# Performance work log

Measured on AMD Instinct MI355X. Metric: run time of the kernel, lower is better.

Reference implementation:

```python
import jax, jax.numpy as jnp
import numpy as np

HEADS = 8
DIM_HEAD = 64
LN_EPS = 1e-5


def _layernorm(x, gamma, beta):
    mu = jnp.mean(x, axis=-1, keepdims=True)
    var = jnp.var(x, axis=-1, keepdims=True)
    return (x - mu) * jax.lax.rsqrt(var + LN_EPS) * gamma + beta


def setup_inputs() -> dict:
    key = jax.random.key(0)
    ks = jax.random.split(key, 5)
    B, N, D = 1, 16384, 512
    return {
        "x": jax.random.normal(ks[0], (B, N, D), dtype=jnp.float32),
        "ln_gamma": jnp.ones((D,), dtype=jnp.float32),
        "ln_beta": jnp.zeros((D,), dtype=jnp.float32),
        "w_qkv": jax.random.normal(ks[1], (D, 3 * D), dtype=jnp.float32) * (D ** -0.5),
        "agent": jax.random.normal(ks[2], (HEADS, 512, DIM_HEAD), dtype=jnp.float32) * (DIM_HEAD ** -0.5),
        "w_out": jax.random.normal(ks[3], (D, D), dtype=jnp.float32) * (D ** -0.5),
        "b_out": jnp.zeros((D,), dtype=jnp.float32),
    }


def reference(x, ln_gamma, ln_beta, w_qkv, agent, w_out, b_out):
    # TransLayer: x + Mask_Agent_Attention(LayerNorm(x))
    B, N, D = x.shape
    xn = _layernorm(x, ln_gamma, ln_beta)

    qkv = xn @ w_qkv                                   # [B, N, 3D]
    q, k, v = jnp.split(qkv, 3, axis=-1)
    # [B, H, N, d]
    q = q.reshape(B, N, HEADS, DIM_HEAD).transpose(0, 2, 1, 3)
    k = k.reshape(B, N, HEADS, DIM_HEAD).transpose(0, 2, 1, 3)
    v = v.reshape(B, N, HEADS, DIM_HEAD).transpose(0, 2, 1, 3)

    scale = DIM_HEAD ** -0.5  # tem=0 -> classical 1/sqrt(d) scaling

    # agents aggregate values: softmax over keys  [B, H, A, N]
    attn1 = jax.nn.softmax(jnp.einsum('had,bhnd->bhan', agent, k) * scale, axis=-1)
    agent_v = jnp.einsum('bhan,bhnd->bhad', attn1, v)  # [B, H, A, d]

    # queries attend to agents: softmax over agents  [B, H, N, A]
    attn2 = jax.nn.softmax(jnp.einsum('bhnd,had->bhna', q, agent) * scale, axis=-1)
    out = jnp.einsum('bhna,bhad->bhnd', attn2, agent_v)  # [B, H, N, d]

    out = out + v  # residual=True: value residual inside attention
    out = out.transpose(0, 2, 1, 3).reshape(B, N, D)
    out = out @ w_out + b_out
    return x + out
```

## Files before the change

kernel.cpp:

```cpp
#include <hip/hip_runtime.h>
#include <stdint.h>

typedef unsigned short u16;
typedef __attribute__((ext_vector_type(8))) short bf16x8;
typedef __attribute__((ext_vector_type(4))) float f32x4;

__device__ __forceinline__ float bf2f(u16 u){
  union { uint32_t i; float f; } v; v.i = ((uint32_t)u) << 16; return v.f;
}
__device__ __forceinline__ u16 f2bf(float f){
  union { float fl; uint32_t i; } v; v.fl = f;
  uint32_t r = v.i + 0x7FFFu + ((v.i >> 16) & 1u);
  return (u16)(r >> 16);
}
__device__ __forceinline__ uint32_t cvt_pk_bf16(float lo, float hi){
  uint32_t r;
  asm("v_cvt_pk_bf16_f32 %0, %1, %2" : "=v"(r) : "v"(lo), "v"(hi));
  return r;
}
__device__ __forceinline__ f32x4 mfma16(bf16x8 a, bf16x8 b, f32x4 c){
  return __builtin_amdgcn_mfma_f32_16x16x32_bf16(a, b, c, 0, 0, 0);
}
__device__ __forceinline__ void gload16(const u16* g, u16* l){
  __builtin_amdgcn_global_load_lds((const __attribute__((address_space(1))) void*)g,
                                   (__attribute__((address_space(3))) void*)l, 16, 0, 0);
}

__global__ __launch_bounds__(256) void k_conv_bf(const float* __restrict__ in, u16* __restrict__ out, int n, float scale){
  int i = (blockIdx.x * 256 + threadIdx.x) * 4;
  if (i >= n) return;
  float4 v = *(const float4*)(in + i);
  ushort4 o; o.x=f2bf(v.x*scale); o.y=f2bf(v.y*scale); o.z=f2bf(v.z*scale); o.w=f2bf(v.w*scale);
  *(ushort4*)(out + i) = o;
}

__global__ __launch_bounds__(256) void k_transp(const float* __restrict__ in, u16* __restrict__ out, int R, int C){
  __shared__ u16 tile[64][68];
  int c0 = blockIdx.x * 64, r0 = blockIdx.y * 64;
  int tr = threadIdx.x >> 4;
  int tc = (threadIdx.x & 15) * 4;
  for (int rr = 0; rr < 4; rr++){
    int r = rr * 16 + tr;
    float4 v = *(const float4*)(in + (size_t)(r0 + r) * C + c0 + tc);
    ushort4 o; o.x=f2bf(v.x); o.y=f2bf(v.y); o.z=f2bf(v.z); o.w=f2bf(v.w);
    *(ushort4*)&tile[r][tc] = o;
  }
  __syncthreads();
  for (int rr = 0; rr < 4; rr++){
    int oc = rr * 16 + tr;
    ushort4 o;
    o.x = tile[tc+0][oc]; o.y = tile[tc+1][oc]; o.z = tile[tc+2][oc]; o.w = tile[tc+3][oc];
    *(ushort4*)(out + (size_t)(c0 + oc) * R + r0 + tc) = o;
  }
}

__global__ __launch_bounds__(128) void k_ln(const float* __restrict__ x, const float* __restrict__ g,
                                            const float* __restrict__ b, u16* __restrict__ xn){
  int row = blockIdx.x;
  int t = threadIdx.x;
  float4 v = *(const float4*)(x + (size_t)row * 512 + t * 4);
  float s = v.x + v.y + v.z + v.w;
  float q = v.x*v.x + v.y*v.y + v.z*v.z + v.w*v.w;
  for (int o = 32; o > 0; o >>= 1){ s += __shfl_down(s, o); q += __shfl_down(q, o); }
  __shared__ float red[4];
  if ((t & 63) == 0){ red[(t >> 6) * 2] = s; red[(t >> 6) * 2 + 1] = q; }
  __syncthreads();
  float mu  = (red[0] + red[2]) * (1.0f/512.0f);
  float var = (red[1] + red[3]) * (1.0f/512.0f) - mu * mu;
  float rs = rsqrtf(var + 1e-5f);
  float4 gv = *(const float4*)(g + t * 4);
  float4 bv = *(const float4*)(b + t * 4);
  ushort4 o;
  o.x = f2bf((v.x - mu) * rs * gv.x + bv.x);
  o.y = f2bf((v.y - mu) * rs * gv.y + bv.y);
  o.z = f2bf((v.z - mu) * rs * gv.z + bv.z);
  o.w = f2bf((v.w - mu) * rs * gv.w + bv.w);
  *(ushort4*)(xn + (size_t)row * 512 + t * 4) = o;
}

__global__ __launch_bounds__(512) void k_gemm_qkv(const u16* __restrict__ A, const u16* __restrict__ Bt,
                                                  u16* __restrict__ C, u16* __restrict__ vT){
  __shared__ u16 aL[2][256 * 64];
  __shared__ u16 bL[2][128 * 64];
  int m0 = blockIdx.x * 256, n0 = blockIdx.y * 128;
  int t = threadIdx.x, w = t >> 6, l = t & 63;
  int wm = (w >> 1) * 64, wn = (w & 1) * 64;
  int lr = l & 15;
  int blkSrc = (l & 7) ^ ((l >> 3) & 7);
  const u16* gA = A  + (size_t)(m0 + w*8 + (l >> 3)) * 512 + blkSrc * 8;
  const u16* gB = Bt + (size_t)(n0 + w*8 + (l >> 3)) * 512 + blkSrc * 8;
  f32x4 acc[4][4];
  for (int i=0;i<4;i++) for (int j=0;j<4;j++) acc[i][j] = {0.f,0.f,0.f,0.f};

  auto stage = [&](int buf, int k0){
    #pragma unroll
    for (int p = 0; p < 4; p++)
      gload16(gA + (size_t)p*64*512 + k0, &aL[buf][(p*64 + w*8) * 64]);
    #pragma unroll
    for (int p = 0; p < 2; p++)
      gload16(gB + (size_t)p*64*512 + k0, &bL[buf][(p*64 + w*8) * 64]);
  };
  auto comp = [&](const u16* ab, const u16* bb){
    #pragma unroll
    for (int kk = 0; kk < 64; kk += 32){
      int xo = (((l >> 4) + (kk >> 3)) ^ (l & 7)) << 3;
      bf16x8 av[4], bv[4];
      #pragma unroll
      for (int mt=0;mt<4;mt++) av[mt] = *(const bf16x8*)&ab[(wm + mt*16 + lr)*64 + xo];
      #pragma unroll
      for (int nt=0;nt<4;nt++) bv[nt] = *(const bf16x8*)&bb[(wn + nt*16 + lr)*64 + xo];
      #pragma unroll
      for (int mt=0;mt<4;mt++)
        #pragma unroll
        for (int nt=0;nt<4;nt++)
          acc[mt][nt] = mfma16(av[mt], bv[nt], acc[mt][nt]);
    }
  };

  stage(0, 0);
  stage(1, 64);
  asm volatile("s_waitcnt vmcnt(6)" ::: "memory");
  __builtin_amdgcn_s_barrier();
  asm volatile("" ::: "memory");
  int cur = 0;
  #pragma unroll
  for (int tk = 0; tk < 8; tk++){
    comp(&aL[cur][0], &bL[cur][0]);
    if (tk < 7){
      __builtin_amdgcn_s_barrier();
      if (tk + 2 < 8){
        stage(cur, (tk + 2) * 64);
        asm volatile("s_waitcnt vmcnt(6)" ::: "memory");
      } else {
        asm volatile("s_waitcnt vmcnt(0)" ::: "memory");
      }
      __builtin_amdgcn_s_barrier();
      asm volatile("" ::: "memory");
    }
    cur ^= 1;
  }

  int rr = (l >> 4) * 4, cc = l & 15;
  bool isV = (n0 >= 1024);
  for (int mt=0;mt<4;mt++) for (int nt=0;nt<4;nt++){
    int r = m0 + wm + mt*16 + rr;
    int c = n0 + wn + nt*16 + cc;
    ushort4 o;
    o.x = f2bf(acc[mt][nt][0]); o.y = f2bf(acc[mt][nt][1]);
    o.z = f2bf(acc[mt][nt][2]); o.w = f2bf(acc[mt][nt][3]);
    C[(size_t)(r+0) * 1536 + c] = o.x;
    C[(size_t)(r+1) * 1536 + c] = o.y;
    C[(size_t)(r+2) * 1536 + c] = o.z;
    C[(size_t)(r+3) * 1536 + c] = o.w;
    if (isV) *(ushort4*)(vT + ((size_t)(c - 1024) << 14) + r) = o;
  }
}

__global__ __launch_bounds__(512) void k_gemm_out(const u16* __restrict__ A, const u16* __restrict__ Bt,
                                                  const float* __restrict__ x, const float* __restrict__ bias,
                                                  float* __restrict__ y){
  __shared__ u16 aL[2][256 * 64];
  __shared__ u16 bL[2][128 * 64];
  int m0 = blockIdx.x * 256, n0 = blockIdx.y * 128;
  int t = threadIdx.x, w = t >> 6, l = t & 63;
  int wm = (w >> 1) * 64, wn = (w & 1) * 64;
  int lr = l & 15;
  int blkSrc = (l & 7) ^ ((l >> 3) & 7);
  const u16* gA = A  + (size_t)(m0 + w*8 + (l >> 3)) * 512 + blkSrc * 8;
  const u16* gB = Bt + (size_t)(n0 + w*8 + (l >> 3)) * 512 + blkSrc * 8;
  f32x4 acc[4][4];
  for (int i=0;i<4;i++) for (int j=0;j<4;j++) acc[i][j] = {0.f,0.f,0.f,0.f};

  auto stage = [&](int buf, int k0){
    #pragma unroll
    for (int p = 0; p < 4; p++)
      gload16(gA + (size_t)p*64*512 + k0, &aL[buf][(p*64 + w*8) * 64]);
    #pragma unroll
    for (int p = 0; p < 2; p++)
      gload16(gB + (size_t)p*64*512 + k0, &bL[buf][(p*64 + w*8) * 64]);
  };
  auto comp = [&](const u16* ab, const u16* bb){
    #pragma unroll
    for (int kk = 0; kk < 64; kk += 32){
      int xo = (((l >> 4) + (kk >> 3)) ^ (l & 7)) << 3;
      bf16x8 av[4], bv[4];
      #pragma unroll
      for (int mt=0;mt<4;mt++) av[mt] = *(const bf16x8*)&ab[(wm + mt*16 + lr)*64 + xo];
      #pragma unroll
      for (int nt=0;nt<4;nt++) bv[nt] = *(const bf16x8*)&bb[(wn + nt*16 + lr)*64 + xo];
      #pragma unroll
      for (int mt=0;mt<4;mt++)
        #pragma unroll
        for (int nt=0;nt<4;nt++)
          acc[mt][nt] = mfma16(av[mt], bv[nt], acc[mt][nt]);
    }
  };

  stage(0, 0);
  stage(1, 64);
  asm volatile("s_waitcnt vmcnt(6)" ::: "memory");
  __builtin_amdgcn_s_barrier();
  asm volatile("" ::: "memory");
  int cur = 0;
  #pragma unroll
  for (int tk = 0; tk < 8; tk++){
    comp(&aL[cur][0], &bL[cur][0]);
    if (tk < 7){
      __builtin_amdgcn_s_barrier();
      if (tk + 2 < 8){
        stage(cur, (tk + 2) * 64);
        asm volatile("s_waitcnt vmcnt(6)" ::: "memory");
      } else {
        asm volatile("s_waitcnt vmcnt(0)" ::: "memory");
      }
      __builtin_amdgcn_s_barrier();
      asm volatile("" ::: "memory");
    }
    cur ^= 1;
  }

  int rr = (l >> 4) * 4, cc = l & 15;
  for (int mt=0;mt<4;mt++) for (int nt=0;nt<4;nt++)
    for (int j=0;j<4;j++){
      int r = m0 + wm + mt*16 + rr + j;
      int c = n0 + wn + nt*16 + cc;
      y[(size_t)r * 512 + c] = acc[mt][nt][j] + bias[c] + x[(size_t)r * 512 + c];
    }
}

__global__ __launch_bounds__(256) void k_agent_agg(const u16* __restrict__ agbf, const u16* __restrict__ qkv,
                                                   const u16* __restrict__ vT,
                                                   float* __restrict__ nump, float* __restrict__ denp){
  int L = blockIdx.x;
  int g = (L >> 6) * 8 + (L & 7);
  int m = (L >> 3) & 7;
  int h = g >> 4, ch = g & 15, a0 = m * 64;

  __shared__ u16 ag[64][68];
  __shared__ u16 kt[64][68];
  __shared__ u16 vt[64][68];
  __shared__ u16 pt[64][68];
  __shared__ float dnf[4][64];
  int t = threadIdx.x, w = t >> 6, l = t & 63;
  int lr = l & 15, q4 = l >> 4;

  int sr = t >> 2, sc = (t & 3) * 16;
  {
    uint4 a0v = *(const uint4*)(agbf + (size_t)(h * 512 + a0 + sr) * 64 + sc);
    uint4 a1v = *(const uint4*)(agbf + (size_t)(h * 512 + a0 + sr) * 64 + sc + 8);
    *(uint4*)&ag[sr][sc]     = a0v;
    *(uint4*)&ag[sr][sc + 8] = a1v;
  }

  size_t nbase = (size_t)ch * 1024;
  const u16* kp = qkv + 512 + h * 64;
  const u16* vp = vT + ((size_t)(h * 64 + sr) << 14);

  f32x4 acc2[4];
  #pragma unroll
  for (int i=0;i<4;i++) acc2[i] = {0.f,0.f,0.f,0.f};
  float den[4] = {0.f,0.f,0.f,0.f};

  for (int sub = 0; sub < 16; sub++){
    size_t n0 = nbase + sub * 64;
    __syncthreads();
    {
      uint4 rk0 = *(const uint4*)(kp + (n0 + sr) * 1536 + sc);
      uint4 rk1 = *(const uint4*)(kp + (n0 + sr) * 1536 + sc + 8);
      uint4 rv0 = *(const uint4*)(vp + n0 + sc);
      uint4 rv1 = *(const uint4*)(vp + n0 + sc + 8);
      *(uint4*)&kt[sr][sc]     = rk0;
      *(uint4*)&kt[sr][sc + 8] = rk1;
      *(uint4*)&vt[sr][sc]     = rv0;
      *(uint4*)&vt[sr][sc + 8] = rv1;
    }
    __syncthreads();

    f32x4 s[4];
    #pragma unroll
    for (int nt=0;nt<4;nt++) s[nt] = {0.f,0.f,0.f,0.f};
    #pragma unroll
    for (int kk = 0; kk < 64; kk += 32){
      int kb = kk + q4 * 8;
      bf16x8 kf = *(const bf16x8*)&kt[w*16 + lr][kb];
      #pragma unroll
      for (int nt=0;nt<4;nt++){
        bf16x8 af = *(const bf16x8*)&ag[nt*16 + lr][kb];
        s[nt] = mfma16(kf, af, s[nt]);
      }
    }
    #pragma unroll
    for (int nt=0;nt<4;nt++){
      float e0 = __builtin_amdgcn_exp2f(s[nt][0]);
      float e1 = __builtin_amdgcn_exp2f(s[nt][1]);
      float e2 = __builtin_amdgcn_exp2f(s[nt][2]);
      float e3 = __builtin_amdgcn_exp2f(s[nt][3]);
      den[nt] += (e0 + e1) + (e2 + e3);
      uint2 o; o.x = cvt_pk_bf16(e0, e1); o.y = cvt_pk_bf16(e2, e3);
      *(uint2*)&pt[nt*16 + lr][w*16 + q4*4] = o;
    }
    __syncthreads();

    #pragma unroll
    for (int kk = 0; kk < 64; kk += 32){
      int kb = kk + q4 * 8;
      bf16x8 vf = *(const bf16x8*)&vt[w*16 + lr][kb];
      #pragma unroll
      for (int mt=0;mt<4;mt++){
        bf16x8 pf = *(const bf16x8*)&pt[mt*16 + lr][kb];
        acc2[mt] = mfma16(pf, vf, acc2[mt]);
      }
    }
  }

  #pragma unroll
  for (int nt=0;nt<4;nt++){
    float r = den[nt];
    r += __shfl_xor(r, 16);
    r += __shfl_xor(r, 32);
    if (q4 == 0) dnf[w][nt*16 + lr] = r;
  }
  __syncthreads();

  size_t base = ((size_t)(h * 16 + ch) * 512 + a0) * 64;
  #pragma unroll
  for (int mt=0;mt<4;mt++)
    #pragma unroll
    for (int j=0;j<4;j++){
      int a = mt*16 + q4*4 + j;
      int d = w*16 + lr;
      nump[base + (size_t)a*64 + d] = acc2[mt][j];
    }
  if (t < 64)
    denp[(size_t)(h*16 + ch) * 512 + a0 + t] = dnf[0][t] + dnf[1][t] + dnf[2][t] + dnf[3][t];
}

__global__ __launch_bounds__(64) void k_agent_reduce(const float* __restrict__ nump, const float* __restrict__ denp,
                                                     u16* __restrict__ avtg){
  int h = blockIdx.x >> 9;
  int a = blockIdx.x & 511;
  int d = threadIdx.x;
  float num = 0.f, den = 0.f;
  for (int c = 0; c < 16; c++){
    num += nump[((size_t)(h * 16 + c) * 512 + a) * 64 + d];
    den += denp[(size_t)(h * 16 + c) * 512 + a];
  }
  avtg[((size_t)h * 64 + d) * 512 + a] = f2bf(num / den);
}

__global__ __launch_bounds__(256) void k_qattn(const u16* __restrict__ qkv, const u16* __restrict__ agbf,
                                               const u16* __restrict__ avtg, u16* __restrict__ atto){
  int n0 = blockIdx.x * 64;
  int h  = blockIdx.y;
  __shared__ u16 agL[2][64][68];
  __shared__ u16 avL[2][64][68];
  __shared__ u16 pt[2][64][68];
  __shared__ float dnf[4][64];
  int t = threadIdx.x, w = t >> 6, l = t & 63;
  int lr = l & 15, q4 = l >> 4;

  bf16x8 qf[4][2];
  #pragma unroll
  for (int nt=0;nt<4;nt++)
    #pragma unroll
    for (int kk=0;kk<2;kk++)
      qf[nt][kk] = *(const bf16x8*)(qkv + (size_t)(n0 + nt*16 + lr) * 1536 + h*64 + kk*32 + q4*8);

  int sr = t >> 2, sc = (t & 3) * 16;
  uint4 rg0, rg1, rv0, rv1;
  rg0 = *(const uint4*)(agbf + (size_t)(h*512 + sr) * 64 + sc);
  rg1 = *(const uint4*)(agbf + (size_t)(h*512 + sr) * 64 + sc + 8);
  rv0 = *(const uint4*)(avtg + (size_t)(h*64 + sr) * 512 + sc);
  rv1 = *(const uint4*)(avtg + (size_t)(h*64 + sr) * 512 + sc + 8);
  *(uint4*)&agL[0][sr][sc]     = rg0;
  *(uint4*)&agL[0][sr][sc + 8] = rg1;
  *(uint4*)&avL[0][sr][sc]     = rv0;
  *(uint4*)&avL[0][sr][sc + 8] = rv1;
  __syncthreads();

  f32x4 acc[4];
  #pragma unroll
  for (int i=0;i<4;i++) acc[i] = {0.f,0.f,0.f,0.f};
  float den[4] = {0.f,0.f,0.f,0.f};

  for (int at = 0; at < 8; at++){
    int cur = at & 1, prv = cur ^ 1;
    if (at + 1 < 8){
      rg0 = *(const uint4*)(agbf + (size_t)(h*512 + (at+1)*64 + sr) * 64 + sc);
      rg1 = *(const uint4*)(agbf + (size_t)(h*512 + (at+1)*64 + sr) * 64 + sc + 8);
      rv0 = *(const uint4*)(avtg + (size_t)(h*64 + sr) * 512 + (at+1)*64 + sc);
      rv1 = *(const uint4*)(avtg + (size_t)(h*64 + sr) * 512 + (at+1)*64 + sc + 8);
    }
    f32x4 s[4];
    #pragma unroll
    for (int nt=0;nt<4;nt++) s[nt] = {0.f,0.f,0.f,0.f};
    #pragma unroll
    for (int kk = 0; kk < 2; kk++){
      bf16x8 af = *(const bf16x8*)&agL[cur][w*16 + lr][kk*32 + q4*8];
      #pragma unroll
      for (int nt=0;nt<4;nt++)
        s[nt] = mfma16(af, qf[nt][kk], s[nt]);
    }
    #pragma unroll
    for (int nt=0;nt<4;nt++){
      float e0 = __builtin_amdgcn_exp2f(s[nt][0]);
      float e1 = __builtin_amdgcn_exp2f(s[nt][1]);
      float e2 = __builtin_amdgcn_exp2f(s[nt][2]);
      float e3 = __builtin_amdgcn_exp2f(s[nt][3]);
      den[nt] += (e0 + e1) + (e2 + e3);
      uint2 o; o.x = cvt_pk_bf16(e0, e1); o.y = cvt_pk_bf16(e2, e3);
      *(uint2*)&pt[cur][nt*16 + lr][w*16 + q4*4] = o;
    }
    if (at > 0){
      #pragma unroll
      for (int kk = 0; kk < 64; kk += 32){
        int kb = kk + q4*8;
        bf16x8 vf = *(const bf16x8*)&avL[prv][w*16 + lr][kb];
        #pragma unroll
        for (int mt=0;mt<4;mt++){
          bf16x8 pf = *(const bf16x8*)&pt[prv][mt*16 + lr][kb];
          acc[mt] = mfma16(pf, vf, acc[mt]);
        }
      }
    }
    __syncthreads();
    if (at + 1 < 8){
      *(uint4*)&agL[prv][sr][sc]     = rg0;
      *(uint4*)&agL[prv][sr][sc + 8] = rg1;
      *(uint4*)&avL[prv][sr][sc]     = rv0;
      *(uint4*)&avL[prv][sr][sc + 8] = rv1;
    }
    __syncthreads();
  }
  {
    #pragma unroll
    for (int kk = 0; kk < 64; kk += 32){
      int kb = kk + q4*8;
      bf16x8 vf = *(const bf16x8*)&avL[1][w*16 + lr][kb];
      #pragma unroll
      for (int mt=0;mt<4;mt++){
        bf16x8 pf = *(const bf16x8*)&pt[1][mt*16 + lr][kb];
        acc[mt] = mfma16(pf, vf, acc[mt]);
      }
    }
  }

  float dq[4];
  #pragma unroll
  for (int nt=0;nt<4;nt++){
    float r = den[nt];
    r += __shfl_xor(r, 16);
    r += __shfl_xor(r, 32);
    dq[nt] = r;
  }
  if (q4 == 0)
    #pragma unroll
    for (int nt=0;nt<4;nt++) dnf[w][nt*16 + lr] = dq[nt];
  __syncthreads();
  if (t < 64){
    float sden = dnf[0][t] + dnf[1][t] + dnf[2][t] + dnf[3][t];
    dnf[0][t] = __builtin_amdgcn_rcpf(sden);
  }
  __syncthreads();

  int d = w*16 + lr;
  #pragma unroll
  for (int mt=0;mt<4;mt++){
    #pragma unroll
    for (int j=0;j<4;j++){
      int n = mt*16 + q4*4 + j;
      float v = bf2f(qkv[(size_t)(n0 + n) * 1536 + 1024 + h * 64 + d]);
      atto[(size_t)(n0 + n) * 512 + h * 64 + d] = f2bf(acc[mt][j] * dnf[0][n] + v);
    }
  }
}

extern "C" void kernel_launch(void* const* d_in, const int* in_sizes, int n_in,
                              void* d_out, int out_size, void* d_ws, size_t ws_size,
                              hipStream_t stream) {
  const float* x     = (const float*)d_in[0];
  const float* gamma = (const float*)d_in[1];
  const float* beta  = (const float*)d_in[2];
  const float* w_qkv = (const float*)d_in[3];
  const float* agent = (const float*)d_in[4];
  const float* w_out = (const float*)d_in[5];
  const float* b_out = (const float*)d_in[6];
  float* y = (float*)d_out;

  char* ws = (char*)d_ws;
  u16*   xn    = (u16*)  (ws + 0);
  u16*   qkv   = (u16*)  (ws + 16777216);
  u16*   wqkvt = (u16*)  (ws + 67108864);
  u16*   woutt = (u16*)  (ws + 68681728);
  u16*   agbf  = (u16*)  (ws + 69206016);
  u16*   avtg  = (u16*)  (ws + 69730304);
  u16*   vT    = (u16*)  (ws + 70254592);
  u16*   atto  = (u16*)  (ws + 70254592);
  float* nump  = (float*)(ws + 87031808);
  float* denp  = (float*)(ws + 103809024);

  k_conv_bf   <<<dim3(256),     dim3(256), 0, stream>>>(agent, agbf, 8*512*64, 0.125f * 1.44269504089f);
  k_transp    <<<dim3(24, 8),   dim3(256), 0, stream>>>(w_qkv, wqkvt, 512, 1536);
  k_transp    <<<dim3(8, 8),    dim3(256), 0, stream>>>(w_out, woutt, 512, 512);
  k_ln        <<<dim3(16384),   dim3(128), 0, stream>>>(x, gamma, beta, xn);
  k_gemm_qkv  <<<dim3(64, 12),  dim3(512), 0, stream>>>(xn, wqkvt, qkv, vT);
  k_agent_agg <<<dim3(1024),    dim3(256), 0, stream>>>(agbf, qkv, vT, nump, denp);
  k_agent_reduce<<<dim3(4096),  dim3(64),  0, stream>>>(nump, denp, avtg);
  k_qattn     <<<dim3(256, 8),  dim3(256), 0, stream>>>(qkv, agbf, avtg, atto);
  k_gemm_out  <<<dim3(64, 4),   dim3(512), 0, stream>>>(atto, woutt, x, b_out, y);
}
```

Measured before the change: 154.8 us.

## Double-buffer K/V tiles in agent aggregation kernel with register prefetch

The agent aggregation kernel now keeps two LDS buffers for the K and V tiles. It loads the next 64-row chunk from global memory into registers before the current chunk's MFMA work, then stores it into the alternate buffer after that work. This removes one barrier per iteration and is meant to hide global load latency behind the compute. The cost is twice the LDS for K/V and higher register pressure, which may lower occupancy.

```diff
diff --git a/kernel.cpp b/kernel.cpp
--- a/kernel.cpp
+++ b/kernel.cpp
@@ -237,8 +237,8 @@
   int h = g >> 4, ch = g & 15, a0 = m * 64;
 
   __shared__ u16 ag[64][68];
-  __shared__ u16 kt[64][68];
-  __shared__ u16 vt[64][68];
+  __shared__ u16 ktL[2][64][68];
+  __shared__ u16 vtL[2][64][68];
   __shared__ u16 pt[64][68];
   __shared__ float dnf[4][64];
   int t = threadIdx.x, w = t >> 6, l = t & 63;
@@ -256,33 +256,40 @@
   const u16* kp = qkv + 512 + h * 64;
   const u16* vp = vT + ((size_t)(h * 64 + sr) << 14);
 
+  {
+    uint4 rk0 = *(const uint4*)(kp + (nbase + sr) * 1536 + sc);
+    uint4 rk1 = *(const uint4*)(kp + (nbase + sr) * 1536 + sc + 8);
+    uint4 rv0 = *(const uint4*)(vp + nbase + sc);
+    uint4 rv1 = *(const uint4*)(vp + nbase + sc + 8);
+    *(uint4*)&ktL[0][sr][sc]     = rk0;
+    *(uint4*)&ktL[0][sr][sc + 8] = rk1;
+    *(uint4*)&vtL[0][sr][sc]     = rv0;
+    *(uint4*)&vtL[0][sr][sc + 8] = rv1;
+  }
+  __syncthreads();
+
   f32x4 acc2[4];
   #pragma unroll
   for (int i=0;i<4;i++) acc2[i] = {0.f,0.f,0.f,0.f};
   float den[4] = {0.f,0.f,0.f,0.f};
 
   for (int sub = 0; sub < 16; sub++){
-    size_t n0 = nbase + sub * 64;
-    __syncthreads();
-    {
-      uint4 rk0 = *(const uint4*)(kp + (n0 + sr) * 1536 + sc);
-      uint4 rk1 = *(const uint4*)(kp + (n0 + sr) * 1536 + sc + 8);
-      uint4 rv0 = *(const uint4*)(vp + n0 + sc);
-      uint4 rv1 = *(const uint4*)(vp + n0 + sc + 8);
-      *(uint4*)&kt[sr][sc]     = rk0;
-      *(uint4*)&kt[sr][sc + 8] = rk1;
-      *(uint4*)&vt[sr][sc]     = rv0;
-      *(uint4*)&vt[sr][sc + 8] = rv1;
-    }
-    __syncthreads();
-
+    int cur = sub & 1, nxt = cur ^ 1;
+    uint4 rk0, rk1, rv0, rv1;
+    if (sub + 1 < 16){
+      size_t n1 = nbase + (sub + 1) * 64;
+      rk0 = *(const uint4*)(kp + (n1 + sr) * 1536 + sc);
+      rk1 = *(const uint4*)(kp + (n1 + sr) * 1536 + sc + 8);
+      rv0 = *(const uint4*)(vp + n1 + sc);
+      rv1 = *(const uint4*)(vp + n1 + sc + 8);
+    }
     f32x4 s[4];
     #pragma unroll
     for (int nt=0;nt<4;nt++) s[nt] = {0.f,0.f,0.f,0.f};
     #pragma unroll
     for (int kk = 0; kk < 64; kk += 32){
       int kb = kk + q4 * 8;
-      bf16x8 kf = *(const bf16x8*)&kt[w*16 + lr][kb];
+      bf16x8 kf = *(const bf16x8*)&ktL[cur][w*16 + lr][kb];
       #pragma unroll
       for (int nt=0;nt<4;nt++){
         bf16x8 af = *(const bf16x8*)&ag[nt*16 + lr][kb];
@@ -304,13 +311,20 @@
     #pragma unroll
     for (int kk = 0; kk < 64; kk += 32){
       int kb = kk + q4 * 8;
-      bf16x8 vf = *(const bf16x8*)&vt[w*16 + lr][kb];
+      bf16x8 vf = *(const bf16x8*)&vtL[cur][w*16 + lr][kb];
       #pragma unroll
       for (int mt=0;mt<4;mt++){
         bf16x8 pf = *(const bf16x8*)&pt[mt*16 + lr][kb];
         acc2[mt] = mfma16(pf, vf, acc2[mt]);
       }
     }
+    if (sub + 1 < 16){
+      *(uint4*)&ktL[nxt][sr][sc]     = rk0;
+      *(uint4*)&ktL[nxt][sr][sc + 8] = rk1;
+      *(uint4*)&vtL[nxt][sr][sc]     = rv0;
+      *(uint4*)&vtL[nxt][sr][sc + 8] = rv1;
+    }
+    __syncthreads();
   }
 
   #pragma unroll
```

New measurement: 155.8 us. About the same (+0.6%).
